# Optimization experiments

Measured on AMD Instinct MI355X. Metric: run time of the kernel, lower is better.

Reference implementation:

```python
import jax, jax.numpy as jnp
import numpy as np

N_SAMPLES = 16384
IN_FEATURES = 2048
N_COMPONENTS = 512
MAX_CROSS_TERMS = 512
# With n_components=512, max_cross_terms=512: interaction_depth=2 -> only pairwise
# cross terms, and n_pairwise = min(512*511//2, 512) = 512 (the first 512 pairs in
# lexicographic (i, j), i<j order -- exactly what the chunked torch loops produce).
_pi, _pj = np.triu_indices(N_COMPONENTS, k=1)  # lexicographic row-major order
PAIR_I = jnp.asarray(_pi[:MAX_CROSS_TERMS])
PAIR_J = jnp.asarray(_pj[:MAX_CROSS_TERMS])
SQRT_EPS = 1e-8


def setup_inputs() -> dict:
    key = jax.random.key(0)
    k1, k2 = jax.random.split(key)
    X = jax.random.normal(k1, (N_SAMPLES, IN_FEATURES), dtype=jnp.float32)
    projection = jax.random.normal(k2, (IN_FEATURES, N_COMPONENTS), dtype=jnp.float32) / np.sqrt(N_COMPONENTS)
    return {"X": X, "projection": projection}


def reference(X, projection):
    # Random projection: [N, in] @ [in, C] -> [N, C]
    Xp = X @ projection
    n = X.shape[0]
    bias = jnp.ones((n, 1), dtype=X.dtype)                 # 'bias' chunk
    p1 = Xp                                                # power_1
    p2 = Xp * Xp                                           # power_2
    p3 = p2 * Xp                                           # power_3
    pairs = Xp[:, PAIR_I] * Xp[:, PAIR_J]                  # pairwise cross terms
    sq = jnp.sqrt(jnp.abs(Xp) + SQRT_EPS)                  # sqrt features
    # Feature layout matches torch offsets: bias | p1 | p2 | p3 | cross | sqrt
    return jnp.concatenate([bias, p1, p2, p3, pairs, sq], axis=1)  # [N, 2561]
```

## Files before the change

### kernel.cpp

```cpp
#include <hip/hip_runtime.h>
#include <hip/hip_bf16.h>
#include <math.h>


typedef __attribute__((ext_vector_type(4))) float f32x4;
typedef __attribute__((ext_vector_type(8))) short bf16x8;

#define MM 16384
#define NN 512
#define KK 2048
#define OUTW 2561

#define BM 128
#define BN 128
#define BK 32
#define KH (KK / 2)
#define NT2 (KH / BK)

__device__ __forceinline__ short f2bf(float x) {
  union { __hip_bfloat16 b; short s; } u;
  u.b = __float2bfloat16(x);
  return u.s;
}

__device__ __forceinline__ bf16x8 cvt8(f32x4 a, f32x4 b) {
  bf16x8 r;
  r[0] = f2bf(a[0]); r[1] = f2bf(a[1]); r[2] = f2bf(a[2]); r[3] = f2bf(a[3]);
  r[4] = f2bf(b[0]); r[5] = f2bf(b[1]); r[6] = f2bf(b[2]); r[7] = f2bf(b[3]);
  return r;
}

__device__ __forceinline__ void gl_lds16(const void* g, void* l) {
  __builtin_amdgcn_global_load_lds((const __attribute__((address_space(1))) unsigned int*)g,
                                   (__attribute__((address_space(3))) unsigned int*)l, 16, 0, 0);
}

__global__ __launch_bounds__(256) void prep_b(const float* __restrict__ P, short* __restrict__ Bt) {
  __shared__ float ts[64][65];
  const int tid = threadIdx.x;
  const int k0 = (blockIdx.x >> 3) * 64;
  const int n0 = (blockIdx.x & 7) * 64;
#pragma unroll
  for (int j = 0; j < 16; ++j) {
    int idx = j * 256 + tid;
    int kr = idx >> 6, nc = idx & 63;
    ts[kr][nc] = P[(size_t)(k0 + kr) * NN + n0 + nc];
  }
  __syncthreads();
#pragma unroll
  for (int j = 0; j < 16; ++j) {
    int idx = j * 256 + tid;
    int nr = idx >> 6, kc = idx & 63;
    Bt[(size_t)(n0 + nr) * KK + k0 + kc] = f2bf(ts[kc][nr]);
  }
}

__global__ __launch_bounds__(256) void gemm8(const float* __restrict__ X,
                                             const short* __restrict__ Bt,
                                             float* __restrict__ out) {
  __shared__ short As[2][BM * BK];
  __shared__ short Bs[2][BN * BK];

  const int tid = threadIdx.x;
  const int wid = tid >> 6, lane = tid & 63;
  const int lrow = lane & 15, kh = lane >> 4;
  const int wr = wid >> 1, wc = wid & 1;

  const int bid = blockIdx.x;
  const int s = (bid & 7) * 128 + (bid >> 3);
  const int ks = s >> 9;
  const int tile = s & 511;
  const int m0 = (tile >> 2) * BM;
  const int n0 = (tile & 3) * BN;
  const int kb = ks * KH;

  const int ar0 = tid >> 2, akq = tid & 3;
  const float* aG = X + (size_t)(m0 + ar0) * KK + kb + akq * 8;
  int aoff[2];
#pragma unroll
  for (int j = 0; j < 2; ++j) {
    int row = j * 64 + ar0;
    aoff[j] = row * 32 + ((akq ^ ((row >> 1) & 3)) << 3);
  }

  const int kd = (lane & 3) ^ ((lane >> 3) & 3);
  const short* bG[2];
  int bOff[2];
#pragma unroll
  for (int p = 0; p < 2; ++p) {
    int R0 = (p * 4 + wid) * 16;
    bOff[p] = R0 * 32;
    bG[p] = Bt + (size_t)(n0 + R0 + (lane >> 2)) * KK + kb + kd * 8;
  }

  f32x4 acc[4][4];
#pragma unroll
  for (int m = 0; m < 4; ++m)
#pragma unroll
    for (int n = 0; n < 4; ++n) acc[m][n] = (f32x4)0.0f;

#pragma unroll
  for (int p = 0; p < 2; ++p) gl_lds16(bG[p], &Bs[0][bOff[p]]);
  f32x4 a0 = *(const f32x4*)aG;
  f32x4 a1 = *(const f32x4*)(aG + 4);
  f32x4 a2 = *(const f32x4*)(aG + (size_t)64 * KK);
  f32x4 a3 = *(const f32x4*)(aG + (size_t)64 * KK + 4);
  *(bf16x8*)&As[0][aoff[0]] = cvt8(a0, a1);
  *(bf16x8*)&As[0][aoff[1]] = cvt8(a2, a3);
  a0 = *(const f32x4*)(aG + BK);
  a1 = *(const f32x4*)(aG + BK + 4);
  a2 = *(const f32x4*)(aG + (size_t)64 * KK + BK);
  a3 = *(const f32x4*)(aG + (size_t)64 * KK + BK + 4);
  __syncthreads();

  int cur = 0;
  for (int t = 0; t < NT2; ++t) {
    if (t + 1 < NT2) {
#pragma unroll
      for (int p = 0; p < 2; ++p) gl_lds16(bG[p] + (size_t)(t + 1) * BK, &Bs[cur ^ 1][bOff[p]]);
      *(bf16x8*)&As[cur ^ 1][aoff[0]] = cvt8(a0, a1);
      *(bf16x8*)&As[cur ^ 1][aoff[1]] = cvt8(a2, a3);
      int t2 = (t + 2 < NT2) ? t + 2 : t;
      const float* ap = aG + (size_t)t2 * BK;
      a0 = *(const f32x4*)ap;
      a1 = *(const f32x4*)(ap + 4);
      a2 = *(const f32x4*)(ap + (size_t)64 * KK);
      a3 = *(const f32x4*)(ap + (size_t)64 * KK + 4);
    }
    const int sw = (lrow >> 1) & 3;
    bf16x8 af[4], bfr[4];
#pragma unroll
    for (int m = 0; m < 4; ++m) {
      int r = wr * 64 + m * 16 + lrow;
      af[m] = *(const bf16x8*)&As[cur][r * 32 + ((kh ^ sw) << 3)];
    }
#pragma unroll
    for (int n = 0; n < 4; ++n) {
      int r = wc * 64 + n * 16 + lrow;
      bfr[n] = *(const bf16x8*)&Bs[cur][r * 32 + ((kh ^ sw) << 3)];
    }
#pragma unroll
    for (int m = 0; m < 4; ++m)
#pragma unroll
      for (int n = 0; n < 4; ++n)
        acc[m][n] = __builtin_amdgcn_mfma_f32_16x16x32_bf16(af[m], bfr[n], acc[m][n], 0, 0, 0);
    __syncthreads();
    cur ^= 1;
  }

#pragma unroll
  for (int m = 0; m < 4; ++m)
#pragma unroll
    for (int n = 0; n < 4; ++n)
#pragma unroll
      for (int r = 0; r < 4; ++r) {
        int row = m0 + wr * 64 + m * 16 + kh * 4 + r;
        int col = n0 + wc * 64 + n * 16 + lrow;
        out[(size_t)row * OUTW + 1 + ks * NN + col] = acc[m][n][r];
      }
}

__global__ __launch_bounds__(512) void epi2_k(float* __restrict__ out) {
  const int r = blockIdx.x;
  const int c = threadIdx.x;
  float* row = out + (size_t)r * OUTW;
  __shared__ float s[NN];
  float xp = row[1 + c] + row[513 + c];
  s[c] = xp;
  __syncthreads();
  float p2 = xp * xp;
  float p3 = p2 * xp;
  float sq = sqrtf(fabsf(xp) + 1e-8f);
  float pr = (c < 511) ? s[0] * s[c + 1] : s[1] * s[2];
  if (c == 0) row[0] = 1.0f;
  row[1 + c] = xp;
  row[513 + c] = p2;
  row[1025 + c] = p3;
  row[1537 + c] = pr;
  row[2049 + c] = sq;
}

#define FBM 128
#define FBN 128
#define FPAD 40

__global__ __launch_bounds__(256) void gemm_k(const float* __restrict__ A,
                                              const float* __restrict__ B,
                                              float* __restrict__ out) {
  __shared__ __align__(16) short Asf[FBM][FPAD];
  __shared__ __align__(16) short Bsf[FBN][FPAD];
  const int tid = threadIdx.x;
  const int bx = blockIdx.x;
  const int m0 = (bx >> 2) * FBM;
  const int n0 = (bx & 3) * FBN;
  const int wid = tid >> 6, lane = tid & 63;
  const int wr = wid >> 1, wc = wid & 1;
  const int lrow = lane & 15, kh = lane >> 4;
  f32x4 acc[4][4];
#pragma unroll
  for (int i = 0; i < 4; i++)
#pragma unroll
    for (int j = 0; j < 4; j++) acc[i][j] = (f32x4)0.0f;
  for (int k0 = 0; k0 < KK; k0 += BK) {
#pragma unroll
    for (int i = 0; i < 4; i++) {
      int fid = i * 256 + tid;
      int ar = fid >> 3, ac = (fid & 7) << 2;
      f32x4 v = *(const f32x4*)(A + (size_t)(m0 + ar) * KK + (k0 + ac));
      short h0 = f2bf(v[0]), h1 = f2bf(v[1]), h2 = f2bf(v[2]), h3 = f2bf(v[3]);
      Asf[ar][ac] = h0; Asf[ar][ac + 1] = h1; Asf[ar][ac + 2] = h2; Asf[ar][ac + 3] = h3;
    }
#pragma unroll
    for (int i = 0; i < 4; i++) {
      int fid = i * 256 + tid;
      int br = fid >> 5, bc = (fid & 31) << 2;
      f32x4 v = *(const f32x4*)(B + (size_t)(k0 + br) * NN + (n0 + bc));
#pragma unroll
      for (int j = 0; j < 4; j++) Bsf[bc + j][br] = f2bf(v[j]);
    }
    __syncthreads();
    bf16x8 af[4], bf[4];
#pragma unroll
    for (int m = 0; m < 4; m++) af[m] = *(const bf16x8*)&Asf[wr * 64 + m * 16 + lrow][kh * 8];
#pragma unroll
    for (int n = 0; n < 4; n++) bf[n] = *(const bf16x8*)&Bsf[wc * 64 + n * 16 + lrow][kh * 8];
#pragma unroll
    for (int m = 0; m < 4; m++)
#pragma unroll
      for (int n = 0; n < 4; n++)
        acc[m][n] = __builtin_amdgcn_mfma_f32_16x16x32_bf16(af[m], bf[n], acc[m][n], 0, 0, 0);
    __syncthreads();
  }
#pragma unroll
  for (int m = 0; m < 4; m++)
#pragma unroll
    for (int n = 0; n < 4; n++)
#pragma unroll
      for (int r = 0; r < 4; r++) {
        int row = m0 + wr * 64 + m * 16 + kh * 4 + r;
        int col = n0 + wc * 64 + n * 16 + lrow;
        out[(size_t)row * OUTW + 1 + col] = acc[m][n][r];
      }
}

__global__ __launch_bounds__(512) void epi_k(float* __restrict__ out) {
  const int r = blockIdx.x;
  const int c = threadIdx.x;
  float* row = out + (size_t)r * OUTW;
  __shared__ float s[NN];
  float xp = row[1 + c];
  s[c] = xp;
  __syncthreads();
  float p2 = xp * xp;
  float p3 = p2 * xp;
  float sq = sqrtf(fabsf(xp) + 1e-8f);
  float pr = (c < 511) ? s[0] * s[c + 1] : s[1] * s[2];
  if (c == 0) row[0] = 1.0f;
  row[513 + c] = p2;
  row[1025 + c] = p3;
  row[1537 + c] = pr;
  row[2049 + c] = sq;
}

extern "C" void kernel_launch(void* const* d_in, const int* in_sizes, int n_in,
                              void* d_out, int out_size, void* d_ws, size_t ws_size,
                              hipStream_t stream) {
  const float* X = (const float*)d_in[0];
  const float* P = (const float*)d_in[1];
  float* out = (float*)d_out;
  (void)in_sizes; (void)n_in; (void)out_size;

  if (ws_size >= (size_t)NN * KK * sizeof(short)) {
    short* Bt = (short*)d_ws;
    prep_b<<<dim3(256), dim3(256), 0, stream>>>(P, Bt);
    gemm8<<<dim3(1024), dim3(256), 0, stream>>>(X, Bt, out);
    epi2_k<<<dim3(MM), dim3(512), 0, stream>>>(out);
  } else {
    gemm_k<<<dim3(512), dim3(256), 0, stream>>>(X, P, out);
    epi_k<<<dim3(MM), dim3(512), 0, stream>>>(out);
  }
}
```

Baseline: 142.2 us.

## Pre-convert X to bf16 in workspace and load both GEMM operands via direct LDS copies

Adds a separate pass that converts X from fp32 to bf16 into the workspace. A new GEMM kernel then streams both A and B tiles with global-to-LDS loads instead of register loads plus in-loop conversion, and declares a higher occupancy hint. This takes conversion work and register staging out of the main loop. In exchange it adds an extra full read of X and a write and re-read of a 64 MB bf16 copy, and this path only runs when the workspace is large enough.

New measurement: 136.3 us. -4.1%, faster.

```diff
diff --git a/kernel.cpp b/kernel.cpp
--- a/kernel.cpp
+++ b/kernel.cpp
@@ -55,9 +55,16 @@
   }
 }
 
-__global__ __launch_bounds__(256) void gemm8(const float* __restrict__ X,
-                                             const short* __restrict__ Bt,
-                                             float* __restrict__ out) {
+__global__ __launch_bounds__(256) void xcvt(const float* __restrict__ X, short* __restrict__ Xb) {
+  size_t i = ((size_t)blockIdx.x * 256 + threadIdx.x) * 8;
+  f32x4 a = *(const f32x4*)(X + i);
+  f32x4 b = *(const f32x4*)(X + i + 4);
+  *(bf16x8*)(Xb + i) = cvt8(a, b);
+}
+
+__global__ __launch_bounds__(256, 4) void gemm9(const short* __restrict__ Xb,
+                                                const short* __restrict__ Bt,
+                                                float* __restrict__ out) {
   __shared__ short As[2][BM * BK];
   __shared__ short Bs[2][BN * BK];
 
@@ -74,6 +81,107 @@
   const int n0 = (tile & 3) * BN;
   const int kb = ks * KH;
 
+  const int kd = (lane & 3) ^ ((lane >> 3) & 3);
+  const short* aG[2];
+  const short* bG[2];
+  int tOff[2];
+#pragma unroll
+  for (int p = 0; p < 2; ++p) {
+    int R0 = (p * 4 + wid) * 16;
+    tOff[p] = R0 * 32;
+    aG[p] = Xb + (size_t)(m0 + R0 + (lane >> 2)) * KK + kb + kd * 8;
+    bG[p] = Bt + (size_t)(n0 + R0 + (lane >> 2)) * KK + kb + kd * 8;
+  }
+
+  f32x4 acc[4][4];
+#pragma unroll
+  for (int m = 0; m < 4; ++m)
+#pragma unroll
+    for (int n = 0; n < 4; ++n) acc[m][n] = (f32x4)0.0f;
+
+#pragma unroll
+  for (int p = 0; p < 2; ++p) gl_lds16(aG[p], &As[0][tOff[p]]);
+#pragma unroll
+  for (int p = 0; p < 2; ++p) gl_lds16(bG[p], &Bs[0][tOff[p]]);
+  __syncthreads();
+
+  int cur = 0;
+  for (int t = 0; t < NT2; ++t) {
+    if (t + 1 < NT2) {
+#pragma unroll
+      for (int p = 0; p < 2; ++p) gl_lds16(aG[p] + (size_t)(t + 1) * BK, &As[cur ^ 1][tOff[p]]);
+#pragma unroll
+      for (int p = 0; p < 2; ++p) gl_lds16(bG[p] + (size_t)(t + 1) * BK, &Bs[cur ^ 1][tOff[p]]);
+    }
+    const int sw = (lrow >> 1) & 3;
+    bf16x8 af[4], bfr[4];
+#pragma unroll
+    for (int m = 0; m < 4; ++m) {
+      int r = wr * 64 + m * 16 + lrow;
+      af[m] = *(const bf16x8*)&As[cur][r * 32 + ((kh ^ sw) << 3)];
+    }
+#pragma unroll
+    for (int n = 0; n < 4; ++n) {
+      int r = wc * 64 + n * 16 + lrow;
+      bfr[n] = *(const bf16x8*)&Bs[cur][r * 32 + ((kh ^ sw) << 3)];
+    }
+#pragma unroll
+    for (int m = 0; m < 4; ++m)
+#pragma unroll
+      for (int n = 0; n < 4; ++n)
+        acc[m][n] = __builtin_amdgcn_mfma_f32_16x16x32_bf16(af[m], bfr[n], acc[m][n], 0, 0, 0);
+    __syncthreads();
+    cur ^= 1;
+  }
+
+#pragma unroll
+  for (int m = 0; m < 4; ++m)
+#pragma unroll
+    for (int n = 0; n < 4; ++n)
+#pragma unroll
+      for (int r = 0; r < 4; ++r) {
+        int row = m0 + wr * 64 + m * 16 + kh * 4 + r;
+        int col = n0 + wc * 64 + n * 16 + lrow;
+        out[(size_t)row * OUTW + 1 + ks * NN + col] = acc[m][n][r];
+      }
+}
+
+__global__ __launch_bounds__(512) void epi2_k(float* __restrict__ out) {
+  const int r = blockIdx.x;
+  const int c = threadIdx.x;
+  float* row = out + (size_t)r * OUTW;
+  __shared__ float s[NN];
+  float xp = row[1 + c] + row[513 + c];
+  s[c] = xp;
+  __syncthreads();
+  float p2 = xp * xp;
+  float p3 = p2 * xp;
+  float sq = sqrtf(fabsf(xp) + 1e-8f);
+  float pr = (c < 511) ? s[0] * s[c + 1] : s[1] * s[2];
+  if (c == 0) row[0] = 1.0f;
+  row[1 + c] = xp;
+  row[513 + c] = p2;
+  row[1025 + c] = p3;
+  row[1537 + c] = pr;
+  row[2049 + c] = sq;
+}
+
+__global__ __launch_bounds__(256) void gemm8(const float* __restrict__ X,
+                                             const short* __restrict__ Bt,
+                                             float* __restrict__ out) {
+  __shared__ short As[2][BM * BK];
+  __shared__ short Bs[2][BN * BK];
+  const int tid = threadIdx.x;
+  const int wid = tid >> 6, lane = tid & 63;
+  const int lrow = lane & 15, kh = lane >> 4;
+  const int wr = wid >> 1, wc = wid & 1;
+  const int bid = blockIdx.x;
+  const int s = (bid & 7) * 128 + (bid >> 3);
+  const int ks = s >> 9;
+  const int tile = s & 511;
+  const int m0 = (tile >> 2) * BM;
+  const int n0 = (tile & 3) * BN;
+  const int kb = ks * KH;
   const int ar0 = tid >> 2, akq = tid & 3;
   const float* aG = X + (size_t)(m0 + ar0) * KK + kb + akq * 8;
   int aoff[2];
@@ -82,7 +190,6 @@
     int row = j * 64 + ar0;
     aoff[j] = row * 32 + ((akq ^ ((row >> 1) & 3)) << 3);
   }
-
   const int kd = (lane & 3) ^ ((lane >> 3) & 3);
   const short* bG[2];
   int bOff[2];
@@ -92,13 +199,11 @@
     bOff[p] = R0 * 32;
     bG[p] = Bt + (size_t)(n0 + R0 + (lane >> 2)) * KK + kb + kd * 8;
   }
-
   f32x4 acc[4][4];
 #pragma unroll
   for (int m = 0; m < 4; ++m)
 #pragma unroll
     for (int n = 0; n < 4; ++n) acc[m][n] = (f32x4)0.0f;
-
 #pragma unroll
   for (int p = 0; p < 2; ++p) gl_lds16(bG[p], &Bs[0][bOff[p]]);
   f32x4 a0 = *(const f32x4*)aG;
@@ -112,7 +217,6 @@
   a2 = *(const f32x4*)(aG + (size_t)64 * KK + BK);
   a3 = *(const f32x4*)(aG + (size_t)64 * KK + BK + 4);
   __syncthreads();
-
   int cur = 0;
   for (int t = 0; t < NT2; ++t) {
     if (t + 1 < NT2) {
@@ -147,7 +251,6 @@
     __syncthreads();
     cur ^= 1;
   }
-
 #pragma unroll
   for (int m = 0; m < 4; ++m)
 #pragma unroll
@@ -158,26 +261,6 @@
         int col = n0 + wc * 64 + n * 16 + lrow;
         out[(size_t)row * OUTW + 1 + ks * NN + col] = acc[m][n][r];
       }
-}
-
-__global__ __launch_bounds__(512) void epi2_k(float* __restrict__ out) {
-  const int r = blockIdx.x;
-  const int c = threadIdx.x;
-  float* row = out + (size_t)r * OUTW;
-  __shared__ float s[NN];
-  float xp = row[1 + c] + row[513 + c];
-  s[c] = xp;
-  __syncthreads();
-  float p2 = xp * xp;
-  float p3 = p2 * xp;
-  float sq = sqrtf(fabsf(xp) + 1e-8f);
-  float pr = (c < 511) ? s[0] * s[c + 1] : s[1] * s[2];
-  if (c == 0) row[0] = 1.0f;
-  row[1 + c] = xp;
-  row[513 + c] = p2;
-  row[1025 + c] = p3;
-  row[1537 + c] = pr;
-  row[2049 + c] = sq;
 }
 
 #define FBM 128
@@ -270,7 +353,17 @@
   float* out = (float*)d_out;
   (void)in_sizes; (void)n_in; (void)out_size;
 
-  if (ws_size >= (size_t)NN * KK * sizeof(short)) {
+  const size_t btBytes = (size_t)NN * KK * sizeof(short);
+  const size_t xbBytes = (size_t)MM * KK * sizeof(short);
+
+  if (ws_size >= btBytes + xbBytes) {
+    short* Bt = (short*)d_ws;
+    short* Xb = (short*)((char*)d_ws + btBytes);
+    prep_b<<<dim3(256), dim3(256), 0, stream>>>(P, Bt);
+    xcvt<<<dim3((MM * KK) / (256 * 8)), dim3(256), 0, stream>>>(X, Xb);
+    gemm9<<<dim3(1024), dim3(256), 0, stream>>>(Xb, Bt, out);
+    epi2_k<<<dim3(MM), dim3(512), 0, stream>>>(out);
+  } else if (ws_size >= btBytes) {
     short* Bt = (short*)d_ws;
     prep_b<<<dim3(256), dim3(256), 0, stream>>>(P, Bt);
     gemm8<<<dim3(1024), dim3(256), 0, stream>>>(X, Bt, out);
```

## Stage fp32 A tiles directly to LDS asynchronously and convert to bf16 at fragment load

Applied to the files above, without the earlier changes.

The GEMM kernel now copies the fp32 X tiles straight into LDS with the async global-to-LDS path, using a swizzled layout, instead of loading them into registers and converting before the LDS store. The fp32-to-bf16 conversion moves to fragment-load time. The main loop becomes a two-stage prefetch pipeline driven by explicit vmcnt waits and raw barriers, and the launch bounds add an occupancy hint. This aims to remove register staging and exposed latency on the A path. In exchange it doubles the LDS footprint for A and repeats the conversion per wave, since each wave converts its own fragments.

After: 139.5 us. Within noise of the previous version (-1.9%).

```diff
diff --git a/kernel.cpp b/kernel.cpp
--- a/kernel.cpp
+++ b/kernel.cpp
@@ -55,10 +55,10 @@
   }
 }
 
-__global__ __launch_bounds__(256) void gemm8(const float* __restrict__ X,
-                                             const short* __restrict__ Bt,
-                                             float* __restrict__ out) {
-  __shared__ short As[2][BM * BK];
+__global__ __launch_bounds__(256, 3) void gemm12(const float* __restrict__ X,
+                                                 const short* __restrict__ Bt,
+                                                 float* __restrict__ out) {
+  __shared__ float Asf[2][BM * BK];
   __shared__ short Bs[2][BN * BK];
 
   const int tid = threadIdx.x;
@@ -74,15 +74,15 @@
   const int n0 = (tile & 3) * BN;
   const int kb = ks * KH;
 
-  const int ar0 = tid >> 2, akq = tid & 3;
-  const float* aG = X + (size_t)(m0 + ar0) * KK + kb + akq * 8;
-  int aoff[2];
-#pragma unroll
-  for (int j = 0; j < 2; ++j) {
-    int row = j * 64 + ar0;
-    aoff[j] = row * 32 + ((akq ^ ((row >> 1) & 3)) << 3);
-  }
-
+  const int aslot = (lane & 7) ^ ((lane >> 3) & 7);
+  const float* aG[4];
+  int aOff[4];
+#pragma unroll
+  for (int q = 0; q < 4; ++q) {
+    int R = (wid * 4 + q) * 8;
+    aOff[q] = R * 32;
+    aG[q] = X + (size_t)(m0 + R + (lane >> 3)) * KK + kb + aslot * 4;
+  }
   const int kd = (lane & 3) ^ ((lane >> 3) & 3);
   const short* bG[2];
   int bOff[2];
@@ -99,54 +99,52 @@
 #pragma unroll
     for (int n = 0; n < 4; ++n) acc[m][n] = (f32x4)0.0f;
 
-#pragma unroll
-  for (int p = 0; p < 2; ++p) gl_lds16(bG[p], &Bs[0][bOff[p]]);
-  f32x4 a0 = *(const f32x4*)aG;
-  f32x4 a1 = *(const f32x4*)(aG + 4);
-  f32x4 a2 = *(const f32x4*)(aG + (size_t)64 * KK);
-  f32x4 a3 = *(const f32x4*)(aG + (size_t)64 * KK + 4);
-  *(bf16x8*)&As[0][aoff[0]] = cvt8(a0, a1);
-  *(bf16x8*)&As[0][aoff[1]] = cvt8(a2, a3);
-  a0 = *(const f32x4*)(aG + BK);
-  a1 = *(const f32x4*)(aG + BK + 4);
-  a2 = *(const f32x4*)(aG + (size_t)64 * KK + BK);
-  a3 = *(const f32x4*)(aG + (size_t)64 * KK + BK + 4);
-  __syncthreads();
-
-  int cur = 0;
-  for (int t = 0; t < NT2; ++t) {
-    if (t + 1 < NT2) {
-#pragma unroll
-      for (int p = 0; p < 2; ++p) gl_lds16(bG[p] + (size_t)(t + 1) * BK, &Bs[cur ^ 1][bOff[p]]);
-      *(bf16x8*)&As[cur ^ 1][aoff[0]] = cvt8(a0, a1);
-      *(bf16x8*)&As[cur ^ 1][aoff[1]] = cvt8(a2, a3);
-      int t2 = (t + 2 < NT2) ? t + 2 : t;
-      const float* ap = aG + (size_t)t2 * BK;
-      a0 = *(const f32x4*)ap;
-      a1 = *(const f32x4*)(ap + 4);
-      a2 = *(const f32x4*)(ap + (size_t)64 * KK);
-      a3 = *(const f32x4*)(ap + (size_t)64 * KK + 4);
-    }
-    const int sw = (lrow >> 1) & 3;
+  auto stage = [&](int t, int b) {
+#pragma unroll
+    for (int q = 0; q < 4; ++q) gl_lds16(aG[q] + (size_t)t * BK, &Asf[b][aOff[q]]);
+#pragma unroll
+    for (int p = 0; p < 2; ++p) gl_lds16(bG[p] + (size_t)t * BK, &Bs[b][bOff[p]]);
+  };
+  auto compute = [&](int b) {
+    const float* ab = &Asf[b][0];
+    const short* bb = &Bs[b][0];
+    const int swb = (lrow >> 1) & 3;
     bf16x8 af[4], bfr[4];
 #pragma unroll
     for (int m = 0; m < 4; ++m) {
       int r = wr * 64 + m * 16 + lrow;
-      af[m] = *(const bf16x8*)&As[cur][r * 32 + ((kh ^ sw) << 3)];
+      f32x4 lo = *(const f32x4*)(ab + r * 32 + (((2 * kh) ^ (r & 7)) << 2));
+      f32x4 hi = *(const f32x4*)(ab + r * 32 + (((2 * kh + 1) ^ (r & 7)) << 2));
+      af[m] = cvt8(lo, hi);
     }
 #pragma unroll
     for (int n = 0; n < 4; ++n) {
       int r = wc * 64 + n * 16 + lrow;
-      bfr[n] = *(const bf16x8*)&Bs[cur][r * 32 + ((kh ^ sw) << 3)];
+      bfr[n] = *(const bf16x8*)(bb + r * 32 + ((kh ^ swb) << 3));
     }
 #pragma unroll
     for (int m = 0; m < 4; ++m)
 #pragma unroll
       for (int n = 0; n < 4; ++n)
         acc[m][n] = __builtin_amdgcn_mfma_f32_16x16x32_bf16(af[m], bfr[n], acc[m][n], 0, 0, 0);
-    __syncthreads();
-    cur ^= 1;
-  }
+  };
+
+  stage(0, 0);
+  stage(1, 1);
+
+  for (int t = 0; t < NT2 - 2; ++t) {
+    asm volatile("s_waitcnt vmcnt(6)" ::: "memory");
+    __builtin_amdgcn_s_barrier();
+    compute(t & 1);
+    __builtin_amdgcn_s_barrier();
+    stage(t + 2, t & 1);
+  }
+  asm volatile("s_waitcnt vmcnt(6)" ::: "memory");
+  __builtin_amdgcn_s_barrier();
+  compute((NT2 - 2) & 1);
+  asm volatile("s_waitcnt vmcnt(0)" ::: "memory");
+  __builtin_amdgcn_s_barrier();
+  compute((NT2 - 1) & 1);
 
 #pragma unroll
   for (int m = 0; m < 4; ++m)
@@ -270,10 +268,12 @@
   float* out = (float*)d_out;
   (void)in_sizes; (void)n_in; (void)out_size;
 
-  if (ws_size >= (size_t)NN * KK * sizeof(short)) {
+  const size_t btBytes = (size_t)NN * KK * sizeof(short);
+
+  if (ws_size >= btBytes) {
     short* Bt = (short*)d_ws;
     prep_b<<<dim3(256), dim3(256), 0, stream>>>(P, Bt);
-    gemm8<<<dim3(1024), dim3(256), 0, stream>>>(X, Bt, out);
+    gemm12<<<dim3(1024), dim3(256), 0, stream>>>(X, Bt, out);
     epi2_k<<<dim3(MM), dim3(512), 0, stream>>>(out);
   } else {
     gemm_k<<<dim3(512), dim3(256), 0, stream>>>(X, P, out);
```
